# Kernel optimization log

Measured on AMD Instinct MI355X. Metric: run time of the kernel, lower is better.

## Reference

```python
import jax, jax.numpy as jnp
import numpy as np

B, S, HID = 1, 2048, 2048
NH, NKV, HD = 16, 4, 128
ROPE_BASE = 10000.0


def _rope(q, k, positions):
    # q: [B,NH,S,HD], k: [B,NKV,S,HD]; rotate-half RoPE
    half = HD // 2
    inv_freq = 1.0 / (ROPE_BASE ** (jnp.arange(half, dtype=jnp.float32) / half))
    ang = positions.astype(jnp.float32)[:, None] * inv_freq  # [S, half]
    cos, sin = jnp.cos(ang), jnp.sin(ang)

    def apply(x):
        x1, x2 = x[..., :half], x[..., half:]
        return jnp.concatenate([x1 * cos - x2 * sin, x1 * sin + x2 * cos], axis=-1)

    return apply(q), apply(k)


def setup_inputs() -> dict:
    key = jax.random.key(0)
    ks = jax.random.split(key, 5)
    hidden_states = jax.random.normal(ks[0], (B, S, HID), dtype=jnp.float32)
    positions = jnp.arange(S, dtype=jnp.int32)
    # additive causal mask (finite large negative instead of -inf)
    mask = jnp.triu(jnp.full((S, S), -1e9, dtype=jnp.float32), k=1)[None, None]
    scale = 0.02
    Wq = jax.random.normal(ks[1], (HID, NH * HD), dtype=jnp.float32) * scale
    Wk = jax.random.normal(ks[2], (HID, NKV * HD), dtype=jnp.float32) * scale
    Wv = jax.random.normal(ks[3], (HID, NKV * HD), dtype=jnp.float32) * scale
    Wo = jax.random.normal(ks[4], (NH * HD, HID), dtype=jnp.float32) * scale
    return {"hidden_states": hidden_states, "positions": positions, "mask": mask,
            "Wq": Wq, "Wk": Wk, "Wv": Wv, "Wo": Wo}


def reference(hidden_states, positions, mask, Wq, Wk, Wv, Wo):
    groups = NH // NKV
    q = (hidden_states @ Wq).reshape(B, S, NH, HD).transpose(0, 2, 1, 3)
    k = (hidden_states @ Wk).reshape(B, S, NKV, HD).transpose(0, 2, 1, 3)
    v = (hidden_states @ Wv).reshape(B, S, NKV, HD).transpose(0, 2, 1, 3)
    q, k = _rope(q, k, positions)
    # GQA: duplicate kv heads (repeat_interleave along head dim)
    k = jnp.repeat(k, groups, axis=1)
    v = jnp.repeat(v, groups, axis=1)
    scale = 1.0 / jnp.sqrt(jnp.float32(HD))
    scores = jnp.einsum('bhqd,bhkd->bhqk', q, k) * scale + mask
    attn = jax.nn.softmax(scores.astype(jnp.float32), axis=-1).astype(q.dtype)
    out = jnp.einsum('bhqk,bhkd->bhqd', attn, v)
    out = out.transpose(0, 2, 1, 3).reshape(B, S, NH * HD)
    output = out @ Wo
    return (output, k, v)
```

## Files before the change

kernel.cpp:

```cpp
#include <hip/hip_runtime.h>
#include <hip/hip_bf16.h>
#include <math.h>

#define S_LEN 2048
#define HID_DIM 2048
#define NH 16
#define NKV 4
#define HD 128

typedef __attribute__((ext_vector_type(8))) short bf16x8;
typedef __attribute__((ext_vector_type(4))) float f32x4;

__device__ inline unsigned short f2bf(float f) {
  unsigned int u = __float_as_uint(f);
  unsigned int r = u + 0x7FFFu + ((u >> 16) & 1u);
  return (unsigned short)(r >> 16);
}

__global__ __launch_bounds__(256) void f32_to_bf16_kernel(
    const float* __restrict__ x, unsigned short* __restrict__ y, int n)
{
  int i = (blockIdx.x * 256 + threadIdx.x) * 4;
  if (i < n) {
    float4 v = *(const float4*)&x[i];
    ushort4 o;
    o.x = f2bf(v.x); o.y = f2bf(v.y); o.z = f2bf(v.z); o.w = f2bf(v.w);
    *(ushort4*)&y[i] = o;
  }
}

__global__ __launch_bounds__(256) void transpose_bf16_kernel(
    const float* __restrict__ W, unsigned short* __restrict__ Wt, int K, int N)
{
  __shared__ float t[32][33];
  int bx = blockIdx.x * 32;
  int by = blockIdx.y * 32;
  int tx = threadIdx.x, ty = threadIdx.y;
  #pragma unroll
  for (int i = 0; i < 32; i += 8)
    t[ty + i][tx] = W[(size_t)(by + ty + i) * N + bx + tx];
  __syncthreads();
  #pragma unroll
  for (int i = 0; i < 32; i += 8)
    Wt[(size_t)(bx + ty + i) * K + by + tx] = f2bf(t[tx][ty + i]);
}

#define GBM 128
#define GBN 128
#define GBK 32

__global__ __launch_bounds__(256) void gemm_bt128(
    const unsigned short* __restrict__ A,
    const unsigned short* __restrict__ Bt,
    float* __restrict__ C, int M, int N, int K)
{
  __shared__ __align__(16) unsigned short As[GBM * GBK];
  __shared__ __align__(16) unsigned short Bs[GBN * GBK];
  int bm = blockIdx.y * GBM;
  int bn = blockIdx.x * GBN;
  int tid = threadIdx.x, lane = tid & 63, wave = tid >> 6;
  int wm = wave >> 1, wn = wave & 1;
  int quad = lane >> 4, lcol = lane & 15;

  f32x4 zero = {0.f, 0.f, 0.f, 0.f};
  f32x4 acc[4][4];
  #pragma unroll
  for (int i = 0; i < 4; i++)
    #pragma unroll
    for (int j = 0; j < 4; j++) acc[i][j] = zero;

  for (int k0 = 0; k0 < K; k0 += GBK) {
    #pragma unroll
    for (int t = 0; t < 2; t++) {
      int c = wave * 128 + t * 64 + lane;
      int row = c >> 2, cs = c & 3;
      __builtin_amdgcn_global_load_lds(
          (const __attribute__((address_space(1))) void*)(A + (size_t)(bm + row) * K + k0 + cs * 8),
          (__attribute__((address_space(3))) void*)(As + (size_t)(wave * 128 + t * 64) * 8),
          16, 0, 0);
      __builtin_amdgcn_global_load_lds(
          (const __attribute__((address_space(1))) void*)(Bt + (size_t)(bn + row) * K + k0 + cs * 8),
          (__attribute__((address_space(3))) void*)(Bs + (size_t)(wave * 128 + t * 64) * 8),
          16, 0, 0);
    }
    __syncthreads();
    bf16x8 af[4], bfv[4];
    #pragma unroll
    for (int mb = 0; mb < 4; mb++)
      af[mb] = *(const bf16x8*)&As[(wm * 64 + mb * 16 + lcol) * GBK + quad * 8];
    #pragma unroll
    for (int nb = 0; nb < 4; nb++)
      bfv[nb] = *(const bf16x8*)&Bs[(wn * 64 + nb * 16 + lcol) * GBK + quad * 8];
    #pragma unroll
    for (int mb = 0; mb < 4; mb++)
      #pragma unroll
      for (int nb = 0; nb < 4; nb++)
        acc[mb][nb] = __builtin_amdgcn_mfma_f32_16x16x32_bf16(af[mb], bfv[nb], acc[mb][nb], 0, 0, 0);
    __syncthreads();
  }
  #pragma unroll
  for (int mb = 0; mb < 4; mb++)
    #pragma unroll
    for (int nb = 0; nb < 4; nb++)
      #pragma unroll
      for (int r = 0; r < 4; r++) {
        int mm = bm + wm * 64 + mb * 16 + quad * 4 + r;
        int nn = bn + wn * 64 + nb * 16 + lcol;
        C[(size_t)mm * N + nn] = acc[mb][nb][r];
      }
}

__global__ __launch_bounds__(256) void rope_kernel(
    const float* __restrict__ qkv_raw,
    const int* __restrict__ positions,
    unsigned short* __restrict__ q_ws,
    unsigned short* __restrict__ k_ws,
    float* __restrict__ outk)
{
  const float QSCALE = 0.08838834764831845f * 1.4426950408889634f;
  int s = blockIdx.x;
  float pos = (float)positions[s];
  const float* row = &qkv_raw[(size_t)s * 3072];
  for (int t = threadIdx.x; t < 20 * 64; t += 256) {
    int ch = t >> 6, j = t & 63;
    float freq = expf(-(float)j * 0.14391156831212787f);
    float ang = pos * freq;
    float sn, c;
    sincosf(ang, &sn, &c);
    if (ch < NH) {
      float x1 = row[ch * HD + j], x2 = row[ch * HD + j + 64];
      float o1 = x1 * c - x2 * sn;
      float o2 = x1 * sn + x2 * c;
      size_t base = ((size_t)ch * S_LEN + s) * HD;
      q_ws[base + j] = f2bf(o1 * QSCALE);
      q_ws[base + j + 64] = f2bf(o2 * QSCALE);
    } else {
      int kv = ch - NH;
      float x1 = row[2048 + kv * HD + j], x2 = row[2048 + kv * HD + j + 64];
      float o1 = x1 * c - x2 * sn;
      float o2 = x1 * sn + x2 * c;
      size_t kbase = ((size_t)kv * S_LEN + s) * HD;
      k_ws[kbase + j] = f2bf(o1);
      k_ws[kbase + j + 64] = f2bf(o2);
      #pragma unroll
      for (int g = 0; g < 4; g++) {
        size_t ob = ((size_t)(kv * 4 + g) * S_LEN + s) * HD;
        outk[ob + j] = o1;
        outk[ob + j + 64] = o2;
      }
    }
  }
}

__global__ __launch_bounds__(256) void prep_v_kernel(
    const float* __restrict__ qkv_raw,
    float* __restrict__ outv,
    unsigned short* __restrict__ vT)
{
  __shared__ float t[32][33];
  int s0 = blockIdx.x * 32, d0 = blockIdx.y * 32, kv = blockIdx.z;
  int tx = threadIdx.x, ty = threadIdx.y;
  #pragma unroll
  for (int i = 0; i < 32; i += 8)
    t[ty + i][tx] = qkv_raw[(size_t)(s0 + ty + i) * 3072 + 2560 + kv * HD + d0 + tx];
  __syncthreads();
  #pragma unroll
  for (int i = 0; i < 32; i += 8) {
    float val = t[ty + i][tx];
    #pragma unroll
    for (int g = 0; g < 4; g++)
      outv[((size_t)(kv * 4 + g) * S_LEN + s0 + ty + i) * HD + d0 + tx] = val;
  }
  #pragma unroll
  for (int i = 0; i < 32; i += 8)
    vT[((size_t)kv * HD + d0 + ty + i) * S_LEN + s0 + tx] = f2bf(t[tx][ty + i]);
}

__device__ inline void stage_k_tile(const unsigned short* kbase, unsigned short* dst,
                                    int wave, int lane) {
  #pragma unroll
  for (int i = 0; i < 4; i++) {
    int row = wave * 16 + i * 4 + (lane >> 4);
    int c = (lane & 15) ^ (row & 7);
    __builtin_amdgcn_global_load_lds(
        (const __attribute__((address_space(1))) void*)(kbase + (size_t)row * HD + c * 8),
        (__attribute__((address_space(3))) void*)(dst + (wave * 16 + i * 4) * 128),
        16, 0, 0);
  }
}

__device__ inline void stage_v_tile(const unsigned short* vbase, unsigned short* dst,
                                    int wave, int lane) {
  #pragma unroll
  for (int i = 0; i < 4; i++) {
    int row = wave * 32 + i * 8 + (lane >> 3);
    int c = (lane & 7) ^ (row & 7);
    __builtin_amdgcn_global_load_lds(
        (const __attribute__((address_space(1))) void*)(vbase + (size_t)row * S_LEN + c * 8),
        (__attribute__((address_space(3))) void*)(dst + (wave * 32 + i * 8) * 64),
        16, 0, 0);
  }
}

#define PLD 72
#define C2F 23.082320654223414f

__global__ __launch_bounds__(256) void flash_attn3(
    const unsigned short* __restrict__ q_ws,
    const unsigned short* __restrict__ k_ws,
    const unsigned short* __restrict__ vT_ws,
    unsigned short* __restrict__ attn_ws)
{
  __shared__ __align__(16) unsigned short Ks[2][64 * 128];
  __shared__ __align__(16) unsigned short Vs[128 * 64];
  __shared__ __align__(16) unsigned short Ps[4][16 * PLD];
  const int b = blockIdx.x;
  const int u = b >> 4, h = b & 15, kvh = h >> 2;
  const int qt = (u < 16) ? (31 - u) : (u - 16);
  const int tid = threadIdx.x, lane = tid & 63, wave = tid >> 6;
  const int quad = lane >> 4, lcol = lane & 15;
  const int qrow = qt * 64 + wave * 16 + lcol;

  const unsigned short* kh = k_ws + (size_t)kvh * S_LEN * HD;
  const unsigned short* vh = vT_ws + (size_t)kvh * HD * S_LEN;

  bf16x8 qf[4];
  {
    const unsigned short* qp = &q_ws[((size_t)h * S_LEN + qrow) * HD + quad * 8];
    #pragma unroll
    for (int st = 0; st < 4; st++) qf[st] = *(const bf16x8*)&qp[st * 32];
  }
  f32x4 zero = {0.f, 0.f, 0.f, 0.f};
  f32x4 o_acc[8];
  #pragma unroll
  for (int i = 0; i < 8; i++) o_acc[i] = zero;
  float l_acc = 0.f;

  stage_k_tile(kh, &Ks[0][0], wave, lane);

  for (int kt = 0; kt <= qt; kt++) {
    int cur = kt & 1;
    __syncthreads();
    stage_v_tile(vh + kt * 64, &Vs[0], wave, lane);
    if (kt < qt) stage_k_tile(kh + (size_t)(kt + 1) * 64 * HD, &Ks[cur ^ 1][0], wave, lane);

    f32x4 sc[4];
    #pragma unroll
    for (int kb = 0; kb < 4; kb++) {
      sc[kb] = zero;
      #pragma unroll
      for (int st = 0; st < 4; st++) {
        int krow = kb * 16 + lcol;
        bf16x8 kf = *(const bf16x8*)&Ks[cur][krow * 128 + (((st * 4 + quad) ^ (lcol & 7)) * 8)];
        sc[kb] = __builtin_amdgcn_mfma_f32_16x16x32_bf16(kf, qf[st], sc[kb], 0, 0, 0);
      }
    }

    float pv[4][4];
    if (kt < qt) {
      #pragma unroll
      for (int kb = 0; kb < 4; kb++)
        #pragma unroll
        for (int r = 0; r < 4; r++) {
          float p = exp2f(sc[kb][r] - C2F);
          pv[kb][r] = p;
          l_acc += p;
        }
    } else {
      #pragma unroll
      for (int kb = 0; kb < 4; kb++)
        #pragma unroll
        for (int r = 0; r < 4; r++) {
          int key = kt * 64 + kb * 16 + quad * 4 + r;
          float p = (key <= qrow) ? exp2f(sc[kb][r] - C2F) : 0.f;
          pv[kb][r] = p;
          l_acc += p;
        }
    }

    unsigned short* myPs = &Ps[wave][0];
    #pragma unroll
    for (int kb = 0; kb < 4; kb++) {
      unsigned int u0 = (__float_as_uint(pv[kb][0]) + 0x8000u) >> 16;
      unsigned int u1 = (__float_as_uint(pv[kb][1]) + 0x8000u) & 0xFFFF0000u;
      unsigned int u2 = (__float_as_uint(pv[kb][2]) + 0x8000u) >> 16;
      unsigned int u3 = (__float_as_uint(pv[kb][3]) + 0x8000u) & 0xFFFF0000u;
      uint2 w2; w2.x = u0 | u1; w2.y = u2 | u3;
      *(uint2*)&myPs[lcol * PLD + kb * 16 + quad * 4] = w2;
    }
    __syncthreads();

    bf16x8 pa0 = *(const bf16x8*)&myPs[lcol * PLD + quad * 8];
    bf16x8 pa1 = *(const bf16x8*)&myPs[lcol * PLD + 32 + quad * 8];
    #pragma unroll
    for (int ob = 0; ob < 8; ob++) {
      int vrow = ob * 16 + lcol, sw = lcol & 7;
      bf16x8 v0 = *(const bf16x8*)&Vs[vrow * 64 + ((quad ^ sw) * 8)];
      bf16x8 v1 = *(const bf16x8*)&Vs[vrow * 64 + (((quad + 4) ^ sw) * 8)];
      o_acc[ob] = __builtin_amdgcn_mfma_f32_16x16x32_bf16(pa0, v0, o_acc[ob], 0, 0, 0);
      o_acc[ob] = __builtin_amdgcn_mfma_f32_16x16x32_bf16(pa1, v1, o_acc[ob], 0, 0, 0);
    }
  }

  float l = l_acc;
  l += __shfl_xor(l, 16);
  l += __shfl_xor(l, 32);
  float l_t[4];
  #pragma unroll
  for (int r = 0; r < 4; r++)
    l_t[r] = __shfl(l, (lane & 48) + quad * 4 + r);
  #pragma unroll
  for (int r = 0; r < 4; r++) {
    float inv = 1.f / l_t[r];
    int row = qt * 64 + wave * 16 + quad * 4 + r;
    #pragma unroll
    for (int ob = 0; ob < 8; ob++)
      attn_ws[(size_t)row * (NH * HD) + h * HD + ob * 16 + lcol] = f2bf(o_acc[ob][r] * inv);
  }
}

extern "C" void kernel_launch(void* const* d_in, const int* in_sizes, int n_in,
                              void* d_out, int out_size, void* d_ws, size_t ws_size,
                              hipStream_t stream)
{
  const float* hidden    = (const float*)d_in[0];
  const int*   positions = (const int*)d_in[1];
  const float* Wq = (const float*)d_in[3];
  const float* Wk = (const float*)d_in[4];
  const float* Wv = (const float*)d_in[5];
  const float* Wo = (const float*)d_in[6];

  float* out  = (float*)d_out;
  float* outk = out + (size_t)S_LEN * HID_DIM;
  float* outv = outk + (size_t)NH * S_LEN * HD;

  char* ws = (char*)d_ws;
  unsigned short* h_bf   = (unsigned short*)(ws);
  unsigned short* WT     = (unsigned short*)(ws + ((size_t)8  << 20));
  unsigned short* WoT    = (unsigned short*)(ws + ((size_t)20 << 20));
  float*          qkvraw = (float*)         (ws + ((size_t)28 << 20));
  unsigned short* q_ws   = (unsigned short*)(ws + ((size_t)52 << 20));
  unsigned short* k_ws   = (unsigned short*)(ws + ((size_t)60 << 20));
  unsigned short* vT_ws  = (unsigned short*)(ws + ((size_t)62 << 20));
  unsigned short* attn   = (unsigned short*)(ws + ((size_t)64 << 20));

  dim3 tb(32, 8);
  f32_to_bf16_kernel<<<4096, 256, 0, stream>>>(hidden, h_bf, S_LEN * HID_DIM);
  transpose_bf16_kernel<<<dim3(64, 64), tb, 0, stream>>>(Wq, WT, HID_DIM, 2048);
  transpose_bf16_kernel<<<dim3(16, 64), tb, 0, stream>>>(Wk, WT + (size_t)2048 * 2048, HID_DIM, 512);
  transpose_bf16_kernel<<<dim3(16, 64), tb, 0, stream>>>(Wv, WT + (size_t)2560 * 2048, HID_DIM, 512);
  transpose_bf16_kernel<<<dim3(64, 64), tb, 0, stream>>>(Wo, WoT, 2048, 2048);

  gemm_bt128<<<dim3(24, 16), 256, 0, stream>>>(h_bf, WT, qkvraw, 2048, 3072, 2048);

  rope_kernel<<<2048, 256, 0, stream>>>(qkvraw, positions, q_ws, k_ws, outk);
  prep_v_kernel<<<dim3(64, 4, 4), tb, 0, stream>>>(qkvraw, outv, vT_ws);

  flash_attn3<<<dim3(512), 256, 0, stream>>>(q_ws, k_ws, vT_ws, attn);

  gemm_bt128<<<dim3(16, 16), 256, 0, stream>>>(attn, WoT, out, 2048, 2048, 2048);
}
```

Measured before the change: 282.3 us.

## Split-K GEMMs with bf16 partials, swizzled LDS, and merged weight transposes

```diff
diff --git a/kernel.cpp b/kernel.cpp
--- a/kernel.cpp
+++ b/kernel.cpp
@@ -15,6 +15,9 @@
   unsigned int u = __float_as_uint(f);
   unsigned int r = u + 0x7FFFu + ((u >> 16) & 1u);
   return (unsigned short)(r >> 16);
+}
+__device__ inline float bf2f(unsigned short u) {
+  return __uint_as_float(((unsigned int)u) << 16);
 }
 
 __global__ __launch_bounds__(256) void f32_to_bf16_kernel(
@@ -29,11 +32,20 @@
   }
 }
 
-__global__ __launch_bounds__(256) void transpose_bf16_kernel(
-    const float* __restrict__ W, unsigned short* __restrict__ Wt, int K, int N)
+__global__ __launch_bounds__(256) void transpose_all(
+    const float* __restrict__ Wq, const float* __restrict__ Wk,
+    const float* __restrict__ Wv, const float* __restrict__ Wo,
+    unsigned short* __restrict__ WT, unsigned short* __restrict__ WoT)
 {
   __shared__ float t[32][33];
+  const int z = blockIdx.z;
+  const float* W; unsigned short* D; int N;
+  if (z == 0)      { W = Wq; D = WT;                          N = 2048; }
+  else if (z == 1) { W = Wk; D = WT + (size_t)2048 * 2048;    N = 512;  }
+  else if (z == 2) { W = Wv; D = WT + (size_t)2560 * 2048;    N = 512;  }
+  else             { W = Wo; D = WoT;                         N = 2048; }
   int bx = blockIdx.x * 32;
+  if (bx >= N) return;
   int by = blockIdx.y * 32;
   int tx = threadIdx.x, ty = threadIdx.y;
   #pragma unroll
@@ -42,25 +54,24 @@
   __syncthreads();
   #pragma unroll
   for (int i = 0; i < 32; i += 8)
-    Wt[(size_t)(bx + ty + i) * K + by + tx] = f2bf(t[tx][ty + i]);
-}
-
-#define GBM 128
-#define GBN 128
-#define GBK 32
-
-__global__ __launch_bounds__(256) void gemm_bt128(
+    D[(size_t)(bx + ty + i) * 2048 + by + tx] = f2bf(t[tx][ty + i]);
+}
+
+#define GBK 64
+
+__global__ __launch_bounds__(256) void gemm_bt_splitk(
     const unsigned short* __restrict__ A,
     const unsigned short* __restrict__ Bt,
-    float* __restrict__ C, int M, int N, int K)
-{
-  __shared__ __align__(16) unsigned short As[GBM * GBK];
-  __shared__ __align__(16) unsigned short Bs[GBN * GBK];
-  int bm = blockIdx.y * GBM;
-  int bn = blockIdx.x * GBN;
-  int tid = threadIdx.x, lane = tid & 63, wave = tid >> 6;
-  int wm = wave >> 1, wn = wave & 1;
-  int quad = lane >> 4, lcol = lane & 15;
+    unsigned short* __restrict__ P,
+    int M, int N, int KF)
+{
+  __shared__ __align__(16) unsigned short As[128 * GBK];
+  __shared__ __align__(16) unsigned short Bs[128 * GBK];
+  const int bm = blockIdx.y * 128, bn = blockIdx.x * 128, z = blockIdx.z;
+  const int Kh = KF >> 1, k0z = z * Kh;
+  const int tid = threadIdx.x, lane = tid & 63, wave = tid >> 6;
+  const int wm = wave >> 1, wn = wave & 1;
+  const int quad = lane >> 4, lcol = lane & 15;
 
   f32x4 zero = {0.f, 0.f, 0.f, 0.f};
   f32x4 acc[4][4];
@@ -69,35 +80,40 @@
     #pragma unroll
     for (int j = 0; j < 4; j++) acc[i][j] = zero;
 
-  for (int k0 = 0; k0 < K; k0 += GBK) {
-    #pragma unroll
-    for (int t = 0; t < 2; t++) {
-      int c = wave * 128 + t * 64 + lane;
-      int row = c >> 2, cs = c & 3;
+  for (int k0 = k0z; k0 < k0z + Kh; k0 += GBK) {
+    #pragma unroll
+    for (int i = 0; i < 4; i++) {
+      int s = wave * 256 + i * 64 + lane;
+      int row = s >> 3, g = (s & 7) ^ (row & 7);
       __builtin_amdgcn_global_load_lds(
-          (const __attribute__((address_space(1))) void*)(A + (size_t)(bm + row) * K + k0 + cs * 8),
-          (__attribute__((address_space(3))) void*)(As + (size_t)(wave * 128 + t * 64) * 8),
+          (const __attribute__((address_space(1))) void*)(A + (size_t)(bm + row) * KF + k0 + g * 8),
+          (__attribute__((address_space(3))) void*)(As + (size_t)(wave * 256 + i * 64) * 8),
           16, 0, 0);
       __builtin_amdgcn_global_load_lds(
-          (const __attribute__((address_space(1))) void*)(Bt + (size_t)(bn + row) * K + k0 + cs * 8),
-          (__attribute__((address_space(3))) void*)(Bs + (size_t)(wave * 128 + t * 64) * 8),
+          (const __attribute__((address_space(1))) void*)(Bt + (size_t)(bn + row) * KF + k0 + g * 8),
+          (__attribute__((address_space(3))) void*)(Bs + (size_t)(wave * 256 + i * 64) * 8),
           16, 0, 0);
     }
     __syncthreads();
-    bf16x8 af[4], bfv[4];
-    #pragma unroll
-    for (int mb = 0; mb < 4; mb++)
-      af[mb] = *(const bf16x8*)&As[(wm * 64 + mb * 16 + lcol) * GBK + quad * 8];
-    #pragma unroll
-    for (int nb = 0; nb < 4; nb++)
-      bfv[nb] = *(const bf16x8*)&Bs[(wn * 64 + nb * 16 + lcol) * GBK + quad * 8];
-    #pragma unroll
-    for (int mb = 0; mb < 4; mb++)
+    #pragma unroll
+    for (int st = 0; st < 2; st++) {
+      bf16x8 af[4], bfv[4];
+      int sw = (st * 4 + quad) ^ (lcol & 7);
+      #pragma unroll
+      for (int mb = 0; mb < 4; mb++)
+        af[mb] = *(const bf16x8*)&As[(wm * 64 + mb * 16 + lcol) * GBK + sw * 8];
       #pragma unroll
       for (int nb = 0; nb < 4; nb++)
-        acc[mb][nb] = __builtin_amdgcn_mfma_f32_16x16x32_bf16(af[mb], bfv[nb], acc[mb][nb], 0, 0, 0);
+        bfv[nb] = *(const bf16x8*)&Bs[(wn * 64 + nb * 16 + lcol) * GBK + sw * 8];
+      #pragma unroll
+      for (int mb = 0; mb < 4; mb++)
+        #pragma unroll
+        for (int nb = 0; nb < 4; nb++)
+          acc[mb][nb] = __builtin_amdgcn_mfma_f32_16x16x32_bf16(af[mb], bfv[nb], acc[mb][nb], 0, 0, 0);
+    }
     __syncthreads();
   }
+  unsigned short* Pz = P + (size_t)z * M * N;
   #pragma unroll
   for (int mb = 0; mb < 4; mb++)
     #pragma unroll
@@ -106,12 +122,35 @@
       for (int r = 0; r < 4; r++) {
         int mm = bm + wm * 64 + mb * 16 + quad * 4 + r;
         int nn = bn + wn * 64 + nb * 16 + lcol;
-        C[(size_t)mm * N + nn] = acc[mb][nb][r];
+        Pz[(size_t)mm * N + nn] = f2bf(acc[mb][nb][r]);
       }
 }
 
+__global__ __launch_bounds__(256) void add_out_kernel(
+    const unsigned short* __restrict__ P0, const unsigned short* __restrict__ P1,
+    float* __restrict__ out, int n)
+{
+  int i = (blockIdx.x * 256 + threadIdx.x) * 8;
+  if (i < n) {
+    uint4 a = *(const uint4*)&P0[i];
+    uint4 b = *(const uint4*)&P1[i];
+    float4 o0, o1;
+    o0.x = __uint_as_float(a.x << 16) + __uint_as_float(b.x << 16);
+    o0.y = __uint_as_float(a.x & 0xFFFF0000u) + __uint_as_float(b.x & 0xFFFF0000u);
+    o0.z = __uint_as_float(a.y << 16) + __uint_as_float(b.y << 16);
+    o0.w = __uint_as_float(a.y & 0xFFFF0000u) + __uint_as_float(b.y & 0xFFFF0000u);
+    o1.x = __uint_as_float(a.z << 16) + __uint_as_float(b.z << 16);
+    o1.y = __uint_as_float(a.z & 0xFFFF0000u) + __uint_as_float(b.z & 0xFFFF0000u);
+    o1.z = __uint_as_float(a.w << 16) + __uint_as_float(b.w << 16);
+    o1.w = __uint_as_float(a.w & 0xFFFF0000u) + __uint_as_float(b.w & 0xFFFF0000u);
+    *(float4*)&out[i] = o0;
+    *(float4*)&out[i + 4] = o1;
+  }
+}
+
 __global__ __launch_bounds__(256) void rope_kernel(
-    const float* __restrict__ qkv_raw,
+    const unsigned short* __restrict__ P0,
+    const unsigned short* __restrict__ P1,
     const int* __restrict__ positions,
     unsigned short* __restrict__ q_ws,
     unsigned short* __restrict__ k_ws,
@@ -120,7 +159,8 @@
   const float QSCALE = 0.08838834764831845f * 1.4426950408889634f;
   int s = blockIdx.x;
   float pos = (float)positions[s];
-  const float* row = &qkv_raw[(size_t)s * 3072];
+  const unsigned short* r0 = &P0[(size_t)s * 3072];
+  const unsigned short* r1 = &P1[(size_t)s * 3072];
   for (int t = threadIdx.x; t < 20 * 64; t += 256) {
     int ch = t >> 6, j = t & 63;
     float freq = expf(-(float)j * 0.14391156831212787f);
@@ -128,7 +168,9 @@
     float sn, c;
     sincosf(ang, &sn, &c);
     if (ch < NH) {
-      float x1 = row[ch * HD + j], x2 = row[ch * HD + j + 64];
+      int i1 = ch * HD + j, i2 = i1 + 64;
+      float x1 = bf2f(r0[i1]) + bf2f(r1[i1]);
+      float x2 = bf2f(r0[i2]) + bf2f(r1[i2]);
       float o1 = x1 * c - x2 * sn;
       float o2 = x1 * sn + x2 * c;
       size_t base = ((size_t)ch * S_LEN + s) * HD;
@@ -136,7 +178,9 @@
       q_ws[base + j + 64] = f2bf(o2 * QSCALE);
     } else {
       int kv = ch - NH;
-      float x1 = row[2048 + kv * HD + j], x2 = row[2048 + kv * HD + j + 64];
+      int i1 = 2048 + kv * HD + j, i2 = i1 + 64;
+      float x1 = bf2f(r0[i1]) + bf2f(r1[i1]);
+      float x2 = bf2f(r0[i2]) + bf2f(r1[i2]);
       float o1 = x1 * c - x2 * sn;
       float o2 = x1 * sn + x2 * c;
       size_t kbase = ((size_t)kv * S_LEN + s) * HD;
@@ -153,7 +197,8 @@
 }
 
 __global__ __launch_bounds__(256) void prep_v_kernel(
-    const float* __restrict__ qkv_raw,
+    const unsigned short* __restrict__ P0,
+    const unsigned short* __restrict__ P1,
     float* __restrict__ outv,
     unsigned short* __restrict__ vT)
 {
@@ -161,8 +206,10 @@
   int s0 = blockIdx.x * 32, d0 = blockIdx.y * 32, kv = blockIdx.z;
   int tx = threadIdx.x, ty = threadIdx.y;
   #pragma unroll
-  for (int i = 0; i < 32; i += 8)
-    t[ty + i][tx] = qkv_raw[(size_t)(s0 + ty + i) * 3072 + 2560 + kv * HD + d0 + tx];
+  for (int i = 0; i < 32; i += 8) {
+    size_t idx = (size_t)(s0 + ty + i) * 3072 + 2560 + kv * HD + d0 + tx;
+    t[ty + i][tx] = bf2f(P0[idx]) + bf2f(P1[idx]);
+  }
   __syncthreads();
   #pragma unroll
   for (int i = 0; i < 32; i += 8) {
@@ -338,25 +385,25 @@
   unsigned short* h_bf   = (unsigned short*)(ws);
   unsigned short* WT     = (unsigned short*)(ws + ((size_t)8  << 20));
   unsigned short* WoT    = (unsigned short*)(ws + ((size_t)20 << 20));
-  float*          qkvraw = (float*)         (ws + ((size_t)28 << 20));
+  unsigned short* qkvP   = (unsigned short*)(ws + ((size_t)28 << 20));
   unsigned short* q_ws   = (unsigned short*)(ws + ((size_t)52 << 20));
   unsigned short* k_ws   = (unsigned short*)(ws + ((size_t)60 << 20));
   unsigned short* vT_ws  = (unsigned short*)(ws + ((size_t)62 << 20));
   unsigned short* attn   = (unsigned short*)(ws + ((size_t)64 << 20));
-
-  dim3 tb(32, 8);
+  unsigned short* outP   = qkvP;
+  unsigned short* qkvP1  = qkvP + (size_t)S_LEN * 3072;
+  unsigned short* outP1  = outP + (size_t)S_LEN * HID_DIM;
+
   f32_to_bf16_kernel<<<4096, 256, 0, stream>>>(hidden, h_bf, S_LEN * HID_DIM);
-  transpose_bf16_kernel<<<dim3(64, 64), tb, 0, stream>>>(Wq, WT, HID_DIM, 2048);
-  transpose_bf16_kernel<<<dim3(16, 64), tb, 0, stream>>>(Wk, WT + (size_t)2048 * 2048, HID_DIM, 512);
-  transpose_bf16_kernel<<<dim3(16, 64), tb, 0, stream>>>(Wv, WT + (size_t)2560 * 2048, HID_DIM, 512);
-  transpose_bf16_kernel<<<dim3(64, 64), tb, 0, stream>>>(Wo, WoT, 2048, 2048);
-
-  gemm_bt128<<<dim3(24, 16), 256, 0, stream>>>(h_bf, WT, qkvraw, 2048, 3072, 2048);
-
-  rope_kernel<<<2048, 256, 0, stream>>>(qkvraw, positions, q_ws, k_ws, outk);
-  prep_v_kernel<<<dim3(64, 4, 4), tb, 0, stream>>>(qkvraw, outv, vT_ws);
+  transpose_all<<<dim3(64, 64, 4), dim3(32, 8), 0, stream>>>(Wq, Wk, Wv, Wo, WT, WoT);
+
+  gemm_bt_splitk<<<dim3(24, 16, 2), 256, 0, stream>>>(h_bf, WT, qkvP, 2048, 3072, 2048);
+
+  rope_kernel<<<2048, 256, 0, stream>>>(qkvP, qkvP1, positions, q_ws, k_ws, outk);
+  prep_v_kernel<<<dim3(64, 4, 4), dim3(32, 8), 0, stream>>>(qkvP, qkvP1, outv, vT_ws);
 
   flash_attn3<<<dim3(512), 256, 0, stream>>>(q_ws, k_ws, vT_ws, attn);
 
-  gemm_bt128<<<dim3(16, 16), 256, 0, stream>>>(attn, WoT, out, 2048, 2048, 2048);
-}
+  gemm_bt_splitk<<<dim3(16, 16, 2), 256, 0, stream>>>(attn, WoT, outP, 2048, 2048, 2048);
+  add_out_kernel<<<2048, 256, 0, stream>>>(outP, outP1, out, S_LEN * HID_DIM);
+}
```

After: 245.1 us. 13.2% less time.
